# Kernel tuning notes

Hardware: AMD Instinct MI355X
Metric: run time of the kernel (lower is better)

## Reference

```python
import jax, jax.numpy as jnp
import numpy as np

B, S, HID = 2, 2048, 2048
H, KVH, D = 16, 2, 256
ROT = 64  # head_dim * partial_rotary_factor (0.25)
EPS = 1e-6


def setup_inputs() -> dict:
    key = jax.random.key(0)
    ks = jax.random.split(key, 6)
    hidden_states = jax.random.normal(ks[0], (B, S, HID), dtype=jnp.float32)
    # real partial-RoPE cos/sin, rope_theta = 1e6
    inv_freq = 1.0 / (1e6 ** (np.arange(0, ROT, 2, dtype=np.float32) / ROT))
    pos = np.arange(S, dtype=np.float32)
    freqs = np.outer(pos, inv_freq)                      # [S, ROT/2]
    emb = np.concatenate([freqs, freqs], axis=-1)        # [S, ROT]
    cos = jnp.broadcast_to(jnp.asarray(np.cos(emb)), (B, S, ROT))
    sin = jnp.broadcast_to(jnp.asarray(np.sin(emb)), (B, S, ROT))
    sc = 0.02
    Wq = jax.random.normal(ks[1], (HID, H * D * 2), dtype=jnp.float32) * sc
    Wk = jax.random.normal(ks[2], (HID, KVH * D), dtype=jnp.float32) * sc
    Wv = jax.random.normal(ks[3], (HID, KVH * D), dtype=jnp.float32) * sc
    Wo = jax.random.normal(ks[4], (H * D, HID), dtype=jnp.float32) * sc
    q_norm_w = jnp.zeros((D,), dtype=jnp.float32)
    k_norm_w = jnp.zeros((D,), dtype=jnp.float32)
    return dict(hidden_states=hidden_states, cos=cos, sin=sin, Wq=Wq, Wk=Wk,
                Wv=Wv, Wo=Wo, q_norm_w=q_norm_w, k_norm_w=k_norm_w)


def _rms_norm(x, w):
    x32 = x.astype(jnp.float32)
    out = x32 * jax.lax.rsqrt(jnp.mean(x32 * x32, axis=-1, keepdims=True) + EPS)
    return (out * (1.0 + w.astype(jnp.float32))).astype(x.dtype)


def _rotate_half(x):
    x1, x2 = jnp.split(x, 2, axis=-1)
    return jnp.concatenate([-x2, x1], axis=-1)


def _apply_rope(x, cos, sin):
    # x: [B,S,N,D]; cos/sin: [B,S,ROT] -> unsqueeze head dim
    c = cos[:, :, None, :]
    s = sin[:, :, None, :]
    x_rot, x_pass = x[..., :ROT], x[..., ROT:]
    x_rot = x_rot * c + _rotate_half(x_rot) * s
    return jnp.concatenate([x_rot, x_pass], axis=-1)


def reference(hidden_states, cos, sin, Wq, Wk, Wv, Wo, q_norm_w, k_norm_w):
    b, s, _ = hidden_states.shape
    # gated Q projection: view as (b,s,H,2D), chunk last dim into query + gate
    qg = (hidden_states @ Wq).reshape(b, s, H, 2 * D)
    q, gate = qg[..., :D], qg[..., D:]
    gate = gate.reshape(b, s, H * D)
    k = (hidden_states @ Wk).reshape(b, s, KVH, D)
    v = (hidden_states @ Wv).reshape(b, s, KVH, D)
    # per-head RMSNorm then partial RoPE
    q = _apply_rope(_rms_norm(q, q_norm_w), cos, sin)
    k = _apply_rope(_rms_norm(k, k_norm_w), cos, sin)
    # GQA: repeat kv heads
    rep = H // KVH
    k = jnp.repeat(k, rep, axis=2)  # [b,s,H,D]
    v = jnp.repeat(v, rep, axis=2)
    # causal SDPA (bsnd layout)
    scale = 1.0 / jnp.sqrt(jnp.asarray(D, dtype=q.dtype))
    scores = jnp.einsum('bqhd,bkhd->bhqk', q, k) * scale
    causal = jnp.tril(jnp.ones((s, s), dtype=bool))
    scores = jnp.where(causal[None, None], scores, jnp.finfo(scores.dtype).min)
    probs = jax.nn.softmax(scores, axis=-1)
    attn = jnp.einsum('bhqk,bkhd->bqhd', probs, v).reshape(b, s, H * D)
    # output gating + projection
    attn = attn * jax.nn.sigmoid(gate)
    return attn @ Wo
```

## Files before the change

kernel.cpp:

```cpp
#include <hip/hip_runtime.h>
#include <cstdint>
#include <cstddef>

#define S_   2048
#define H_   16
#define KVH_ 2
#define D_   256

typedef __attribute__((ext_vector_type(4))) float          float4v;
typedef __attribute__((ext_vector_type(4))) float          floatx4;
typedef __attribute__((ext_vector_type(8))) unsigned short ushort8v;
typedef __attribute__((ext_vector_type(4))) unsigned short ushort4v;
typedef __attribute__((ext_vector_type(8))) short          short8;

__device__ __forceinline__ float bf2f(unsigned short u){
  union{float f; unsigned int i;} v; v.i = ((unsigned int)u)<<16; return v.f;
}
__device__ __forceinline__ unsigned short f2bf(float f){
  union{float f; unsigned int i;} v; v.f = f;
  unsigned int r = v.i + 0x7FFFu + ((v.i>>16)&1u);
  return (unsigned short)(r>>16);
}
__device__ __forceinline__ void gld16(const void* g, void* l){
  __builtin_amdgcn_global_load_lds(
      (const __attribute__((address_space(1))) unsigned int*)g,
      (__attribute__((address_space(3))) unsigned int*)l, 16, 0, 0);
}

__global__ __launch_bounds__(256) void conv_k(
    const float* __restrict__ in, unsigned short* __restrict__ out)
{
  const size_t i = ((size_t)blockIdx.x*256 + threadIdx.x)*8;
  float4v a0 = *(const float4v*)(in + i), a1 = *(const float4v*)(in + i + 4);
  ushort8v u;
#pragma unroll
  for (int e=0;e<4;e++){ u[e]=f2bf(a0[e]); u[e+4]=f2bf(a1[e]); }
  *(ushort8v*)(out + i) = u;
}

__global__ __launch_bounds__(256) void tconv_k(
    const float* __restrict__ in, unsigned short* __restrict__ out, int K, int N)
{
  __shared__ unsigned short T[64][72];
  const int n0 = blockIdx.x<<6, k0 = blockIdx.y<<6;
  const int t = threadIdx.x, r = t>>2, c = (t&3)<<4;
  const float* ip = in + (size_t)(k0+r)*N + n0 + c;
  float4v a0=*(const float4v*)ip,     a1=*(const float4v*)(ip+4);
  float4v a2=*(const float4v*)(ip+8), a3=*(const float4v*)(ip+12);
  ushort8v u0,u1;
#pragma unroll
  for (int e=0;e<4;e++){ u0[e]=f2bf(a0[e]); u0[e+4]=f2bf(a1[e]);
                         u1[e]=f2bf(a2[e]); u1[e+4]=f2bf(a3[e]); }
  *(ushort8v*)&T[r][c] = u0; *(ushort8v*)&T[r][c+8] = u1;
  __syncthreads();
  ushort8v o0,o1;
#pragma unroll
  for (int j=0;j<8;j++){ o0[j]=T[c+j][r]; o1[j]=T[c+8+j][r]; }
  unsigned short* op = out + (size_t)(n0+r)*K + k0 + c;
  *(ushort8v*)op = o0; *(ushort8v*)(op+8) = o1;
}

template<int MODE>
__global__ __launch_bounds__(256,2) void gemm_k(
    const unsigned short* __restrict__ A, const unsigned short* __restrict__ Bt,
    void* __restrict__ out0, void* __restrict__ out1, int K, int N)
{
  __shared__ unsigned short Ash[128*32];
  __shared__ unsigned short Bsh[128*32];
  const int tid  = threadIdx.x;
  const int gm   = blockIdx.y<<7, gn = blockIdx.x<<7;
  const int lane = tid & 63, wave = tid >> 6;
  const int quad = lane >> 4, col = lane & 15;
  const int wm   = (wave>>1)<<6, wn = (wave&1)<<6;
  const int rowoff = lane>>2;
  const int chunk  = (lane&3) ^ (rowoff&3);
  const int ra0 = wave<<4, ra1 = 64 + (wave<<4);
  const unsigned short* Ab = A  + (size_t)gm*K;
  const unsigned short* Bb = Bt + (size_t)gn*K;
  const int cf = (quad ^ (col&3))<<3;

  floatx4 acc[4][4];
#pragma unroll
  for (int i=0;i<4;i++)
#pragma unroll
    for (int j=0;j<4;j++) acc[i][j] = (floatx4)0.f;

  for (int kk=0; kk<K; kk+=32){
    __syncthreads();
    {
      const int ko = kk + chunk*8;
      gld16(Ab + (size_t)(ra0+rowoff)*K + ko, &Ash[ra0*32]);
      gld16(Ab + (size_t)(ra1+rowoff)*K + ko, &Ash[ra1*32]);
      gld16(Bb + (size_t)(ra0+rowoff)*K + ko, &Bsh[ra0*32]);
      gld16(Bb + (size_t)(ra1+rowoff)*K + ko, &Bsh[ra1*32]);
    }
    __syncthreads();
    short8 af[4], bfr[4];
#pragma unroll
    for (int mi=0;mi<4;mi++) af[mi]  = *(const short8*)&Ash[(wm+mi*16+col)*32 + cf];
#pragma unroll
    for (int ni=0;ni<4;ni++) bfr[ni] = *(const short8*)&Bsh[(wn+ni*16+col)*32 + cf];
#pragma unroll
    for (int mi=0;mi<4;mi++)
#pragma unroll
      for (int ni=0;ni<4;ni++)
        acc[mi][ni] = __builtin_amdgcn_mfma_f32_16x16x32_bf16(af[mi], bfr[ni], acc[mi][ni], 0,0,0);
  }

#pragma unroll
  for (int mi=0;mi<4;mi++){
#pragma unroll
    for (int r=0;r<4;r++){
      const int m = gm + wm + mi*16 + quad*4 + r;
      const int b = m >> 11, s = m & 2047;
#pragma unroll
      for (int ni=0;ni<4;ni++){
        const int n = gn + wn + ni*16 + col;
        const float v = acc[mi][ni][r];
        if (MODE==0){
          if (n < 8192){
            const int h = n >> 9, dd = n & 511;
            if (dd < 256)
              ((unsigned short*)out0)[(((size_t)b*H_ + h)*S_ + s)*D_ + dd] = f2bf(v);
            else
              ((unsigned short*)out1)[((size_t)m*H_ + h)*D_ + (dd-256)] = f2bf(v);
          } else {
            const int n2 = n - 8192;
            if (n2 < 512){
              const int kvh = n2 >> 8, dd = n2 & 255;
              ((unsigned short*)out0)[(size_t)(67108864/2) + (((size_t)b*KVH_ + kvh)*S_ + s)*D_ + dd] = f2bf(v);
            } else {
              const int nv2 = n2 - 512;
              const int kvh = nv2 >> 8, dd = nv2 & 255;
              ((unsigned short*)out0)[(size_t)(71303168/2) + ((((size_t)b*KVH_ + kvh)*64 + (s>>5))*256 + dd)*32 + (s&31)] = f2bf(v);
            }
          }
        } else {
          ((float*)out0)[(size_t)m*N + n] = v;
        }
      }
    }
  }
}

__global__ __launch_bounds__(256,2) void normrope_k(
    unsigned short* __restrict__ x, const float* __restrict__ w,
    const float* __restrict__ cosp, const float* __restrict__ sinp, int heads)
{
  const int lane = threadIdx.x & 63;
  const int row  = blockIdx.x*4 + (threadIdx.x>>6);
  const int s    = row & (S_-1);
  const int b    = (row / S_) / heads;
  unsigned short* xp = x + (size_t)row * D_;
  const int d = lane*4;
  ushort4v xv = *(const ushort4v*)(xp + d);
  float v0=bf2f(xv[0]), v1=bf2f(xv[1]), v2=bf2f(xv[2]), v3=bf2f(xv[3]);
  float ss = v0*v0+v1*v1+v2*v2+v3*v3;
#pragma unroll
  for (int off=1; off<64; off<<=1) ss += __shfl_xor(ss, off, 64);
  const float rstd = rsqrtf(ss*(1.f/256.f) + 1e-6f);
  float nv[4] = { v0*rstd*(1.f+w[d]),   v1*rstd*(1.f+w[d+1]),
                  v2*rstd*(1.f+w[d+2]), v3*rstd*(1.f+w[d+3]) };
  float ov[4];
#pragma unroll
  for (int j=0;j<4;j++){
    const float other = __shfl_xor(nv[j], 8, 64);
    float o = nv[j];
    if (lane < 16){
      const float c  = cosp[((size_t)b*S_+s)*64 + d + j];
      const float sn = sinp[((size_t)b*S_+s)*64 + d + j];
      o = (lane < 8) ? (nv[j]*c - other*sn) : (nv[j]*c + other*sn);
    }
    ov[j] = o;
  }
  ushort4v ou;
#pragma unroll
  for (int j=0;j<4;j++) ou[j] = f2bf(ov[j]);
  *(ushort4v*)(xp + d) = ou;
}

__global__ __launch_bounds__(256,2) void flash_k(
    const unsigned short* __restrict__ qb, const unsigned short* __restrict__ kbp,
    const unsigned short* __restrict__ vtp, const unsigned short* __restrict__ gb,
    unsigned short* __restrict__ ob)
{
  __shared__ unsigned short SH[2*8192 + 2*8192 + 4*2*640];
  unsigned short* Kb0 = SH;
  unsigned short* Vb0 = SH + 16384;
  const int gid = blockIdx.x;
  const int g   = (gid>>1)&3;
  const int b   = g>>1, kvh = g&1;
  const int idx = ((gid&1)<<6) | (gid>>3);
  const int h   = (kvh<<3) | (idx&7);
  const int qt  = 15 - (idx>>3);
  const int tid = threadIdx.x, wave = tid>>6, lane = tid&63;
  const int quad = lane>>4, col = lane&15;
  const int qw = qt*128 + wave*32;
  unsigned short* Psh = SH + 32768 + wave*1280;

  int kOff[4], vOff[4];
#pragma unroll
  for (int j=0;j<4;j++){
    const int krow = wave*8 + j*2 + (lane>>5);
    kOff[j] = krow*256 + ((lane&31) ^ (krow&7))*8;
    const int vrow = wave*64 + j*16 + (lane>>2);
    vOff[j] = vrow*32 + ((lane&3) ^ (vrow&3))*8;
  }

  short8 qf[2][8];
#pragma unroll
  for (int m=0;m<2;m++){
    const unsigned short* qr = qb + (((size_t)b*H_ + h)*S_ + (qw + m*16 + col))*D_;
#pragma unroll
    for (int dc=0; dc<8; ++dc) qf[m][dc] = *(const short8*)(qr + dc*32 + quad*8);
  }
  floatx4 O[2][16];
#pragma unroll
  for (int m=0;m<2;m++)
#pragma unroll
    for (int i=0;i<16;i++) O[m][i] = (floatx4)0.f;
  float lacc[2][4] = {{0.f,0.f,0.f,0.f},{0.f,0.f,0.f,0.f}};

  const unsigned short* Kg = kbp + ((size_t)b*KVH_ + kvh)*S_*D_;
  const unsigned short* Vg = vtp + ((size_t)b*KVH_ + kvh)*S_*D_;
  const int nch = 4*qt + 4;

#pragma unroll
  for (int j=0;j<4;j++){
    gld16(Kg + kOff[j], Kb0 + wave*2048 + j*512);
    gld16(Vg + vOff[j], Vb0 + wave*2048 + j*512);
  }

  int buf = 0;
  for (int kc=0; kc<nch; ++kc){
    __syncthreads();
    if (kc+1 < nch){
      const unsigned short* kg = Kg + (size_t)(kc+1)*8192;
      const unsigned short* vg = Vg + (size_t)(kc+1)*8192;
      unsigned short* kl = Kb0 + (buf^1)*8192 + wave*2048;
      unsigned short* vl = Vb0 + (buf^1)*8192 + wave*2048;
#pragma unroll
      for (int j=0;j<4;j++){
        gld16(kg + kOff[j], kl + j*512);
        gld16(vg + vOff[j], vl + j*512);
      }
    }
    const unsigned short* Ksh = Kb0 + buf*8192;
    const unsigned short* Vt  = Vb0 + buf*8192;

    floatx4 sc[2][2];
#pragma unroll
    for (int m=0;m<2;m++){ sc[m][0]=(floatx4)0.f; sc[m][1]=(floatx4)0.f; }
#pragma unroll
    for (int dc=0; dc<8; ++dc){
#pragma unroll
      for (int nt=0;nt<2;nt++){
        const int row = nt*16+col;
        short8 kf = *(const short8*)&Ksh[row*256 + (((dc*4+quad) ^ (row&7))<<3)];
        sc[0][nt] = __builtin_amdgcn_mfma_f32_16x16x32_bf16(qf[0][dc], kf, sc[0][nt], 0,0,0);
        sc[1][nt] = __builtin_amdgcn_mfma_f32_16x16x32_bf16(qf[1][dc], kf, sc[1][nt], 0,0,0);
      }
    }
    short8 pf[2];
#pragma unroll
    for (int m=0;m<2;m++){
#pragma unroll
      for (int r=0;r<4;r++){
        const int q = qw + m*16 + quad*4 + r;
        float psum = 0.f;
#pragma unroll
        for (int nt=0;nt<2;nt++){
          const int kv = kc*32 + nt*16 + col;
          const float p = (kv<=q) ? __expf(sc[m][nt][r]*0.0625f) : 0.f;
          psum += p;
          Psh[m*640 + (quad*4+r)*40 + nt*16 + col] = f2bf(p);
        }
        lacc[m][r] += psum;
      }
      pf[m] = *(const short8*)&Psh[m*640 + col*40 + quad*8];
    }
#pragma unroll
    for (int nc=0;nc<16;nc++){
      const int row = nc*16+col;
      short8 vf = *(const short8*)&Vt[row*32 + ((quad ^ (row&3))<<3)];
      O[0][nc] = __builtin_amdgcn_mfma_f32_16x16x32_bf16(pf[0], vf, O[0][nc], 0,0,0);
      O[1][nc] = __builtin_amdgcn_mfma_f32_16x16x32_bf16(pf[1], vf, O[1][nc], 0,0,0);
    }
    buf ^= 1;
  }

  __syncthreads();
  unsigned short* rep = SH + wave*8192;
#pragma unroll
  for (int m=0;m<2;m++){
#pragma unroll
    for (int r=0;r<4;r++){
      float s = lacc[m][r];
      s += __shfl_xor(s,1,64); s += __shfl_xor(s,2,64);
      s += __shfl_xor(s,4,64); s += __shfl_xor(s,8,64);
      const float inv = 1.f/s;
      const int rrow = (m*16 + quad*4 + r)*256;
#pragma unroll
      for (int nc=0;nc<16;nc++)
        rep[rrow + nc*16 + col] = f2bf(O[m][nc][r]*inv);
    }
  }
#pragma unroll
  for (int j=0;j<16;j++){
    const int e  = j*512 + lane*8;
    const int ql = j*2 + (lane>>5);
    const int d  = (lane&31)*8;
    ushort8v ov = *(const ushort8v*)&rep[e];
    const size_t base = (((size_t)b*S_ + (qt*128 + wave*32 + ql))*H_ + h)*D_ + d;
    ushort8v gv = *(const ushort8v*)(gb + base);
    ushort8v w;
#pragma unroll
    for (int k=0;k<8;k++){
      const float gvf = bf2f(gv[k]);
      const float sg  = 1.f/(1.f + __expf(-gvf));
      w[k] = f2bf(bf2f(ov[k])*sg);
    }
    *(ushort8v*)(ob + base) = w;
  }
}

extern "C" void kernel_launch(void* const* d_in, const int* in_sizes, int n_in,
                              void* d_out, int out_size, void* d_ws, size_t ws_size,
                              hipStream_t stream)
{
  const float* hs   = (const float*)d_in[0];
  const float* cosp = (const float*)d_in[1];
  const float* sinp = (const float*)d_in[2];
  const float* Wq   = (const float*)d_in[3];
  const float* Wk   = (const float*)d_in[4];
  const float* Wv   = (const float*)d_in[5];
  const float* Wo   = (const float*)d_in[6];
  const float* qw   = (const float*)d_in[7];
  const float* kw   = (const float*)d_in[8];
  float* out = (float*)d_out;

  char* w = (char*)d_ws;
  unsigned short* q_bf  = (unsigned short*)(w);
  unsigned short* gate  = (unsigned short*)(w + 33554432);
  unsigned short* k_bf  = (unsigned short*)(w + 67108864);
  unsigned short* v_t   = (unsigned short*)(w + 71303168);
  unsigned short* hs_bf = (unsigned short*)(w + 75497472);
  unsigned short* wq_t  = (unsigned short*)(w + 92274688);
  unsigned short* wkv_t = (unsigned short*)(w + 125829120);
  unsigned short* wo_t  = (unsigned short*)(w + 92274688);
  unsigned short* attn  = gate;

  conv_k<<<4096, 256, 0, stream>>>(hs, hs_bf);
  tconv_k<<<dim3(128,32), 256, 0, stream>>>(Wq, wq_t, 2048, 8192);
  tconv_k<<<dim3(8,32),   256, 0, stream>>>(Wk, wkv_t, 2048, 512);
  tconv_k<<<dim3(8,32),   256, 0, stream>>>(Wv, wkv_t + (size_t)512*2048, 2048, 512);
  gemm_k<0><<<dim3(72,32), 256, 0, stream>>>(hs_bf, wq_t, q_bf, gate, 2048, 9216);
  tconv_k<<<dim3(32,64), 256, 0, stream>>>(Wo, wo_t, 4096, 2048);
  normrope_k<<<(2*H_*S_)/4,   256, 0, stream>>>(q_bf, qw, cosp, sinp, H_);
  normrope_k<<<(2*KVH_*S_)/4, 256, 0, stream>>>(k_bf, kw, cosp, sinp, KVH_);
  flash_k<<<dim3(512), 256, 0, stream>>>(q_bf, k_bf, v_t, gate, attn);
  gemm_k<3><<<dim3(16,32), 256, 0, stream>>>(attn, wo_t, out, nullptr, 4096, 2048);
}
```

Measured before the change: 630.5 us.

## Double-buffer GEMM LDS tiles, swap grid order, pair causal q-tiles in flash

The GEMM now double-buffers its A/B LDS tiles, prefetching the next K slice while the current one is used, which drops one barrier per iteration. Its grid axes are swapped so M tiles vary fastest across blocks, changing which blocks share weight tiles in cache. The flash kernel now runs on 256 blocks, and each block handles q-tile p and then 15-p, balancing causal work per block. The cost is twice the GEMM shared memory, which may limit occupancy, and half as many flash blocks in flight.

```diff
diff --git a/kernel.cpp b/kernel.cpp
--- a/kernel.cpp
+++ b/kernel.cpp
@@ -65,10 +65,10 @@
     const unsigned short* __restrict__ A, const unsigned short* __restrict__ Bt,
     void* __restrict__ out0, void* __restrict__ out1, int K, int N)
 {
-  __shared__ unsigned short Ash[128*32];
-  __shared__ unsigned short Bsh[128*32];
+  __shared__ unsigned short Ash[2][128*32];
+  __shared__ unsigned short Bsh[2][128*32];
   const int tid  = threadIdx.x;
-  const int gm   = blockIdx.y<<7, gn = blockIdx.x<<7;
+  const int gm   = blockIdx.x<<7, gn = blockIdx.y<<7;
   const int lane = tid & 63, wave = tid >> 6;
   const int quad = lane >> 4, col = lane & 15;
   const int wm   = (wave>>1)<<6, wn = (wave&1)<<6;
@@ -85,21 +85,29 @@
 #pragma unroll
     for (int j=0;j<4;j++) acc[i][j] = (floatx4)0.f;
 
-  for (int kk=0; kk<K; kk+=32){
+  const int niter = K>>5;
+  {
+    const int ko = chunk*8;
+    gld16(Ab + (size_t)(ra0+rowoff)*K + ko, &Ash[0][ra0*32]);
+    gld16(Ab + (size_t)(ra1+rowoff)*K + ko, &Ash[0][ra1*32]);
+    gld16(Bb + (size_t)(ra0+rowoff)*K + ko, &Bsh[0][ra0*32]);
+    gld16(Bb + (size_t)(ra1+rowoff)*K + ko, &Bsh[0][ra1*32]);
+  }
+  for (int it=0; it<niter; ++it){
+    const int buf = it&1;
     __syncthreads();
-    {
-      const int ko = kk + chunk*8;
-      gld16(Ab + (size_t)(ra0+rowoff)*K + ko, &Ash[ra0*32]);
-      gld16(Ab + (size_t)(ra1+rowoff)*K + ko, &Ash[ra1*32]);
-      gld16(Bb + (size_t)(ra0+rowoff)*K + ko, &Bsh[ra0*32]);
-      gld16(Bb + (size_t)(ra1+rowoff)*K + ko, &Bsh[ra1*32]);
-    }
-    __syncthreads();
+    if (it+1 < niter){
+      const int ko = (it+1)*32 + chunk*8;
+      gld16(Ab + (size_t)(ra0+rowoff)*K + ko, &Ash[buf^1][ra0*32]);
+      gld16(Ab + (size_t)(ra1+rowoff)*K + ko, &Ash[buf^1][ra1*32]);
+      gld16(Bb + (size_t)(ra0+rowoff)*K + ko, &Bsh[buf^1][ra0*32]);
+      gld16(Bb + (size_t)(ra1+rowoff)*K + ko, &Bsh[buf^1][ra1*32]);
+    }
     short8 af[4], bfr[4];
 #pragma unroll
-    for (int mi=0;mi<4;mi++) af[mi]  = *(const short8*)&Ash[(wm+mi*16+col)*32 + cf];
-#pragma unroll
-    for (int ni=0;ni<4;ni++) bfr[ni] = *(const short8*)&Bsh[(wn+ni*16+col)*32 + cf];
+    for (int mi=0;mi<4;mi++) af[mi]  = *(const short8*)&Ash[buf][(wm+mi*16+col)*32 + cf];
+#pragma unroll
+    for (int ni=0;ni<4;ni++) bfr[ni] = *(const short8*)&Bsh[buf][(wn+ni*16+col)*32 + cf];
 #pragma unroll
     for (int mi=0;mi<4;mi++)
 #pragma unroll
@@ -188,14 +196,12 @@
   unsigned short* Kb0 = SH;
   unsigned short* Vb0 = SH + 16384;
   const int gid = blockIdx.x;
-  const int g   = (gid>>1)&3;
-  const int b   = g>>1, kvh = g&1;
-  const int idx = ((gid&1)<<6) | (gid>>3);
-  const int h   = (kvh<<3) | (idx&7);
-  const int qt  = 15 - (idx>>3);
+  const int p   = gid & 7;
+  const int h   = (gid>>3) & 15;
+  const int b   = gid >> 7;
+  const int kvh = h >> 3;
   const int tid = threadIdx.x, wave = tid>>6, lane = tid&63;
   const int quad = lane>>4, col = lane&15;
-  const int qw = qt*128 + wave*32;
   unsigned short* Psh = SH + 32768 + wave*1280;
 
   int kOff[4], vOff[4];
@@ -206,121 +212,126 @@
     const int vrow = wave*64 + j*16 + (lane>>2);
     vOff[j] = vrow*32 + ((lane&3) ^ (vrow&3))*8;
   }
-
-  short8 qf[2][8];
-#pragma unroll
-  for (int m=0;m<2;m++){
-    const unsigned short* qr = qb + (((size_t)b*H_ + h)*S_ + (qw + m*16 + col))*D_;
-#pragma unroll
-    for (int dc=0; dc<8; ++dc) qf[m][dc] = *(const short8*)(qr + dc*32 + quad*8);
-  }
-  floatx4 O[2][16];
-#pragma unroll
-  for (int m=0;m<2;m++)
-#pragma unroll
-    for (int i=0;i<16;i++) O[m][i] = (floatx4)0.f;
-  float lacc[2][4] = {{0.f,0.f,0.f,0.f},{0.f,0.f,0.f,0.f}};
-
   const unsigned short* Kg = kbp + ((size_t)b*KVH_ + kvh)*S_*D_;
   const unsigned short* Vg = vtp + ((size_t)b*KVH_ + kvh)*S_*D_;
-  const int nch = 4*qt + 4;
-
-#pragma unroll
-  for (int j=0;j<4;j++){
-    gld16(Kg + kOff[j], Kb0 + wave*2048 + j*512);
-    gld16(Vg + vOff[j], Vb0 + wave*2048 + j*512);
-  }
-
-  int buf = 0;
-  for (int kc=0; kc<nch; ++kc){
+
+  for (int sp=0; sp<2; ++sp){
+    const int qt = sp ? (15-p) : p;
+    const int qw = qt*128 + wave*32;
+    const int nch = 4*qt + 4;
+
+    short8 qf[2][8];
+#pragma unroll
+    for (int m=0;m<2;m++){
+      const unsigned short* qr = qb + (((size_t)b*H_ + h)*S_ + (qw + m*16 + col))*D_;
+#pragma unroll
+      for (int dc=0; dc<8; ++dc) qf[m][dc] = *(const short8*)(qr + dc*32 + quad*8);
+    }
+    floatx4 O[2][16];
+#pragma unroll
+    for (int m=0;m<2;m++)
+#pragma unroll
+      for (int i=0;i<16;i++) O[m][i] = (floatx4)0.f;
+    float lacc[2][4] = {{0.f,0.f,0.f,0.f},{0.f,0.f,0.f,0.f}};
+
     __syncthreads();
-    if (kc+1 < nch){
-      const unsigned short* kg = Kg + (size_t)(kc+1)*8192;
-      const unsigned short* vg = Vg + (size_t)(kc+1)*8192;
-      unsigned short* kl = Kb0 + (buf^1)*8192 + wave*2048;
-      unsigned short* vl = Vb0 + (buf^1)*8192 + wave*2048;
-#pragma unroll
-      for (int j=0;j<4;j++){
-        gld16(kg + kOff[j], kl + j*512);
-        gld16(vg + vOff[j], vl + j*512);
-      }
-    }
-    const unsigned short* Ksh = Kb0 + buf*8192;
-    const unsigned short* Vt  = Vb0 + buf*8192;
-
-    floatx4 sc[2][2];
-#pragma unroll
-    for (int m=0;m<2;m++){ sc[m][0]=(floatx4)0.f; sc[m][1]=(floatx4)0.f; }
-#pragma unroll
-    for (int dc=0; dc<8; ++dc){
-#pragma unroll
-      for (int nt=0;nt<2;nt++){
-        const int row = nt*16+col;
-        short8 kf = *(const short8*)&Ksh[row*256 + (((dc*4+quad) ^ (row&7))<<3)];
-        sc[0][nt] = __builtin_amdgcn_mfma_f32_16x16x32_bf16(qf[0][dc], kf, sc[0][nt], 0,0,0);
-        sc[1][nt] = __builtin_amdgcn_mfma_f32_16x16x32_bf16(qf[1][dc], kf, sc[1][nt], 0,0,0);
-      }
-    }
-    short8 pf[2];
+#pragma unroll
+    for (int j=0;j<4;j++){
+      gld16(Kg + kOff[j], Kb0 + wave*2048 + j*512);
+      gld16(Vg + vOff[j], Vb0 + wave*2048 + j*512);
+    }
+
+    int buf = 0;
+    for (int kc=0; kc<nch; ++kc){
+      __syncthreads();
+      if (kc+1 < nch){
+        const unsigned short* kg = Kg + (size_t)(kc+1)*8192;
+        const unsigned short* vg = Vg + (size_t)(kc+1)*8192;
+        unsigned short* kl = Kb0 + (buf^1)*8192 + wave*2048;
+        unsigned short* vl = Vb0 + (buf^1)*8192 + wave*2048;
+#pragma unroll
+        for (int j=0;j<4;j++){
+          gld16(kg + kOff[j], kl + j*512);
+          gld16(vg + vOff[j], vl + j*512);
+        }
+      }
+      const unsigned short* Ksh = Kb0 + buf*8192;
+      const unsigned short* Vt  = Vb0 + buf*8192;
+
+      floatx4 sc[2][2];
+#pragma unroll
+      for (int m=0;m<2;m++){ sc[m][0]=(floatx4)0.f; sc[m][1]=(floatx4)0.f; }
+#pragma unroll
+      for (int dc=0; dc<8; ++dc){
+#pragma unroll
+        for (int nt=0;nt<2;nt++){
+          const int row = nt*16+col;
+          short8 kf = *(const short8*)&Ksh[row*256 + (((dc*4+quad) ^ (row&7))<<3)];
+          sc[0][nt] = __builtin_amdgcn_mfma_f32_16x16x32_bf16(qf[0][dc], kf, sc[0][nt], 0,0,0);
+          sc[1][nt] = __builtin_amdgcn_mfma_f32_16x16x32_bf16(qf[1][dc], kf, sc[1][nt], 0,0,0);
+        }
+      }
+      short8 pf[2];
+#pragma unroll
+      for (int m=0;m<2;m++){
+#pragma unroll
+        for (int r=0;r<4;r++){
+          const int q = qw + m*16 + quad*4 + r;
+          float psum = 0.f;
+#pragma unroll
+          for (int nt=0;nt<2;nt++){
+            const int kv = kc*32 + nt*16 + col;
+            const float pv = (kv<=q) ? __expf(sc[m][nt][r]*0.0625f) : 0.f;
+            psum += pv;
+            Psh[m*640 + (quad*4+r)*40 + nt*16 + col] = f2bf(pv);
+          }
+          lacc[m][r] += psum;
+        }
+        pf[m] = *(const short8*)&Psh[m*640 + col*40 + quad*8];
+      }
+#pragma unroll
+      for (int nc=0;nc<16;nc++){
+        const int row = nc*16+col;
+        short8 vf = *(const short8*)&Vt[row*32 + ((quad ^ (row&3))<<3)];
+        O[0][nc] = __builtin_amdgcn_mfma_f32_16x16x32_bf16(pf[0], vf, O[0][nc], 0,0,0);
+        O[1][nc] = __builtin_amdgcn_mfma_f32_16x16x32_bf16(pf[1], vf, O[1][nc], 0,0,0);
+      }
+      buf ^= 1;
+    }
+
+    __syncthreads();
+    unsigned short* rep = SH + wave*8192;
 #pragma unroll
     for (int m=0;m<2;m++){
 #pragma unroll
       for (int r=0;r<4;r++){
-        const int q = qw + m*16 + quad*4 + r;
-        float psum = 0.f;
-#pragma unroll
-        for (int nt=0;nt<2;nt++){
-          const int kv = kc*32 + nt*16 + col;
-          const float p = (kv<=q) ? __expf(sc[m][nt][r]*0.0625f) : 0.f;
-          psum += p;
-          Psh[m*640 + (quad*4+r)*40 + nt*16 + col] = f2bf(p);
-        }
-        lacc[m][r] += psum;
-      }
-      pf[m] = *(const short8*)&Psh[m*640 + col*40 + quad*8];
-    }
-#pragma unroll
-    for (int nc=0;nc<16;nc++){
-      const int row = nc*16+col;
-      short8 vf = *(const short8*)&Vt[row*32 + ((quad ^ (row&3))<<3)];
-      O[0][nc] = __builtin_amdgcn_mfma_f32_16x16x32_bf16(pf[0], vf, O[0][nc], 0,0,0);
-      O[1][nc] = __builtin_amdgcn_mfma_f32_16x16x32_bf16(pf[1], vf, O[1][nc], 0,0,0);
-    }
-    buf ^= 1;
-  }
-
-  __syncthreads();
-  unsigned short* rep = SH + wave*8192;
-#pragma unroll
-  for (int m=0;m<2;m++){
-#pragma unroll
-    for (int r=0;r<4;r++){
-      float s = lacc[m][r];
-      s += __shfl_xor(s,1,64); s += __shfl_xor(s,2,64);
-      s += __shfl_xor(s,4,64); s += __shfl_xor(s,8,64);
-      const float inv = 1.f/s;
-      const int rrow = (m*16 + quad*4 + r)*256;
-#pragma unroll
-      for (int nc=0;nc<16;nc++)
-        rep[rrow + nc*16 + col] = f2bf(O[m][nc][r]*inv);
-    }
-  }
-#pragma unroll
-  for (int j=0;j<16;j++){
-    const int e  = j*512 + lane*8;
-    const int ql = j*2 + (lane>>5);
-    const int d  = (lane&31)*8;
-    ushort8v ov = *(const ushort8v*)&rep[e];
-    const size_t base = (((size_t)b*S_ + (qt*128 + wave*32 + ql))*H_ + h)*D_ + d;
-    ushort8v gv = *(const ushort8v*)(gb + base);
-    ushort8v w;
-#pragma unroll
-    for (int k=0;k<8;k++){
-      const float gvf = bf2f(gv[k]);
-      const float sg  = 1.f/(1.f + __expf(-gvf));
-      w[k] = f2bf(bf2f(ov[k])*sg);
-    }
-    *(ushort8v*)(ob + base) = w;
+        float s = lacc[m][r];
+        s += __shfl_xor(s,1,64); s += __shfl_xor(s,2,64);
+        s += __shfl_xor(s,4,64); s += __shfl_xor(s,8,64);
+        const float inv = 1.f/s;
+        const int rrow = (m*16 + quad*4 + r)*256;
+#pragma unroll
+        for (int nc=0;nc<16;nc++)
+          rep[rrow + nc*16 + col] = f2bf(O[m][nc][r]*inv);
+      }
+    }
+#pragma unroll
+    for (int j=0;j<16;j++){
+      const int e  = j*512 + lane*8;
+      const int ql = j*2 + (lane>>5);
+      const int d  = (lane&31)*8;
+      ushort8v ov = *(const ushort8v*)&rep[e];
+      const size_t base = (((size_t)b*S_ + (qt*128 + wave*32 + ql))*H_ + h)*D_ + d;
+      ushort8v gv = *(const ushort8v*)(gb + base);
+      ushort8v wv;
+#pragma unroll
+      for (int k=0;k<8;k++){
+        const float gvf = bf2f(gv[k]);
+        const float sg  = 1.f/(1.f + __expf(-gvf));
+        wv[k] = f2bf(bf2f(ov[k])*sg);
+      }
+      *(ushort8v*)(ob + base) = wv;
+    }
   }
 }
 
@@ -354,10 +365,10 @@
   tconv_k<<<dim3(128,32), 256, 0, stream>>>(Wq, wq_t, 2048, 8192);
   tconv_k<<<dim3(8,32),   256, 0, stream>>>(Wk, wkv_t, 2048, 512);
   tconv_k<<<dim3(8,32),   256, 0, stream>>>(Wv, wkv_t + (size_t)512*2048, 2048, 512);
-  gemm_k<0><<<dim3(72,32), 256, 0, stream>>>(hs_bf, wq_t, q_bf, gate, 2048, 9216);
+  gemm_k<0><<<dim3(32,72), 256, 0, stream>>>(hs_bf, wq_t, q_bf, gate, 2048, 9216);
   tconv_k<<<dim3(32,64), 256, 0, stream>>>(Wo, wo_t, 4096, 2048);
   normrope_k<<<(2*H_*S_)/4,   256, 0, stream>>>(q_bf, qw, cosp, sinp, H_);
   normrope_k<<<(2*KVH_*S_)/4, 256, 0, stream>>>(k_bf, kw, cosp, sinp, KVH_);
-  flash_k<<<dim3(512), 256, 0, stream>>>(q_bf, k_bf, v_t, gate, attn);
-  gemm_k<3><<<dim3(16,32), 256, 0, stream>>>(attn, wo_t, out, nullptr, 4096, 2048);
-}
+  flash_k<<<dim3(256), 256, 0, stream>>>(q_bf, k_bf, v_t, gate, attn);
+  gemm_k<3><<<dim3(32,16), 256, 0, stream>>>(attn, wo_t, out, nullptr, 4096, 2048);
+}
```

Measured after the change: 709.6 us. 12.5% more time.
